# Kernel tuning notes

Hardware: AMD Instinct MI355X
Metric: run time of the kernel (lower is better)

The kernel has to match this reference:

```python
import jax, jax.numpy as jnp
import numpy as np

B, D, H, T, F = 2, 256, 8, 128, 64
C = H * F          # channels = 512
TE = 512           # time_embed_dim


def setup_inputs() -> dict:
    key = jax.random.key(0)
    ks = jax.random.split(key, 9)
    pd = jax.random.randint(ks[2], (B, T, T), 0, 2 * T - 1, dtype=jnp.int32) - (T - 1)
    s = 0.02
    return {
        "qk": jax.random.normal(ks[0], (B, D, H, T, F), jnp.float32),
        "temb": jax.random.normal(ks[1], (B, T, TE), jnp.float32),
        "pairwise_distances": pd,
        "w_dist": jax.random.normal(ks[3], (3, C), jnp.float32) * s,
        "b_dist": jax.random.normal(ks[4], (C,), jnp.float32) * s,
        "w_time": jax.random.normal(ks[5], (TE, C), jnp.float32) * s,
        "b_time": jax.random.normal(ks[6], (C,), jnp.float32) * s,
        "w_out": jax.random.normal(ks[7], (C, C), jnp.float32) * s,
        "b_out": jax.random.normal(ks[8], (C,), jnp.float32) * s,
    }


def _rpe_net(temb, pd, w_dist, b_dist, w_time, b_time, w_out, b_out):
    d = pd.astype(jnp.float32)
    # (B, T, S, 3): log(1+d+), log(1+d-), indicator(d==0)
    dist_embs = jnp.stack(
        [jnp.log1p(jnp.maximum(d, 0.0)),
         jnp.log1p(jnp.maximum(-d, 0.0)),
         (pd == 0).astype(jnp.float32)],
        axis=-1,
    )
    emb = (temb @ w_time + b_time)[:, :, None, :] + dist_embs @ w_dist + b_dist  # (B,T,S,C)
    R = jax.nn.silu(emb) @ w_out + b_out  # (B,T,S,C)
    return R.reshape(*pd.shape, H, F)     # (B,T,S,H,F)


def reference(qk, temb, pairwise_distances, w_dist, b_dist, w_time, b_time, w_out, b_out):
    R = _rpe_net(temb, pairwise_distances, w_dist, b_dist, w_time, b_time, w_out, b_out)
    # forward_qk: contract head_dim f for every (t, s) pair
    return jnp.einsum('bdhtf,btshf->bdhts', qk, R)
```

## Files before the change

kernel.cpp:

```cpp
#include <hip/hip_runtime.h>
#include <hip/hip_bf16.h>

#define B_  2
#define D_  256
#define H_  8
#define T_  128
#define S_  128
#define F_  64
#define C_  512
#define TE_ 512

typedef _Float16 f16x8 __attribute__((ext_vector_type(8)));
typedef _Float16 f16x4 __attribute__((ext_vector_type(4)));
typedef float    f32x4 __attribute__((ext_vector_type(4)));

__global__ __launch_bounds__(256) void k_time_proj(
    const float* __restrict__ temb, const float* __restrict__ w_time,
    const float* __restrict__ b_time, const float* __restrict__ b_dist,
    float* __restrict__ tp)
{
    int row0 = blockIdx.x * 2;
    int tid  = threadIdx.x;
    __shared__ float te[2][TE_];
    for (int i = tid; i < 2 * TE_; i += 256)
        te[i >> 9][i & 511] = temb[(size_t)row0 * TE_ + i];
    __syncthreads();
    for (int half = 0; half < 2; ++half) {
        int c = tid + half * 256;
        float bias = b_time[c] + b_dist[c];
        float a0 = bias, a1 = bias;
        for (int e = 0; e < TE_; ++e) {
            float w = w_time[(size_t)e * C_ + c];
            a0 += te[0][e] * w;
            a1 += te[1][e] * w;
        }
        tp[(size_t)row0 * C_ + c]       = a0;
        tp[(size_t)(row0 + 1) * C_ + c] = a1;
    }
}

__global__ __launch_bounds__(128) void k_embed_silu(
    const float* __restrict__ tp, const int* __restrict__ pd,
    const float* __restrict__ w_dist, _Float16* __restrict__ A)
{
    int row = blockIdx.x;
    int bt  = row >> 7;
    int d   = pd[row];
    float f0 = log1pf(fmaxf((float)d, 0.f));
    float f1 = log1pf(fmaxf((float)(-d), 0.f));
    float f2 = (d == 0) ? 1.f : 0.f;
    int c0 = threadIdx.x * 4;
    float4 t4 = *(const float4*)&tp[(size_t)bt * C_ + c0];
    float4 w0 = *(const float4*)&w_dist[c0];
    float4 w1 = *(const float4*)&w_dist[C_ + c0];
    float4 w2 = *(const float4*)&w_dist[2 * C_ + c0];
    float e0 = t4.x + f0 * w0.x + f1 * w1.x + f2 * w2.x;
    float e1 = t4.y + f0 * w0.y + f1 * w1.y + f2 * w2.y;
    float e2 = t4.z + f0 * w0.z + f1 * w1.z + f2 * w2.z;
    float e3 = t4.w + f0 * w0.w + f1 * w1.w + f2 * w2.w;
    f16x4 v;
    v.x = (_Float16)(e0 / (1.f + expf(-e0)));
    v.y = (_Float16)(e1 / (1.f + expf(-e1)));
    v.z = (_Float16)(e2 / (1.f + expf(-e2)));
    v.w = (_Float16)(e3 / (1.f + expf(-e3)));
    *(f16x4*)&A[(size_t)row * C_ + c0] = v;
}

__global__ __launch_bounds__(512) void k_wt(
    const float* __restrict__ w_out, _Float16* __restrict__ Wt)
{
    int n = blockIdx.x;
    int k = threadIdx.x;
    Wt[(size_t)n * C_ + k] = (_Float16)w_out[(size_t)k * C_ + n];
}

__global__ __launch_bounds__(256) void k_gemm_R(
    const _Float16* __restrict__ A, const _Float16* __restrict__ Wt,
    const float* __restrict__ b_out, _Float16* __restrict__ R)
{
    const int K = 512, N = 512;
    __shared__ _Float16 As[128][72];
    __shared__ _Float16 Bs[128][72];
    int bm = blockIdx.x, bn = blockIdx.y;
    int tid = threadIdx.x;
    int wave = tid >> 6, lane = tid & 63;
    int wm = (wave >> 1) * 64, wn = (wave & 1) * 64;
    int mrow = lane & 15, kq = (lane >> 4) * 8;
    int lrow = tid >> 3, lcol = (tid & 7) * 8;
    const size_t arow0 = (size_t)bm * 128;
    f32x4 acc[4][4] = {};
    for (int k0 = 0; k0 < K; k0 += 64) {
#pragma unroll
        for (int p = 0; p < 4; ++p) {
            int r = p * 32 + lrow;
            *(f16x8*)&As[r][lcol] = *(const f16x8*)&A[(arow0 + r) * K + k0 + lcol];
            *(f16x8*)&Bs[r][lcol] = *(const f16x8*)&Wt[(size_t)(bn * 128 + r) * K + k0 + lcol];
        }
        __syncthreads();
#pragma unroll
        for (int ks = 0; ks < 64; ks += 32) {
            f16x8 af[4], bfr[4];
#pragma unroll
            for (int i = 0; i < 4; ++i) af[i]  = *(const f16x8*)&As[wm + i * 16 + mrow][ks + kq];
#pragma unroll
            for (int j = 0; j < 4; ++j) bfr[j] = *(const f16x8*)&Bs[wn + j * 16 + mrow][ks + kq];
#pragma unroll
            for (int i = 0; i < 4; ++i)
#pragma unroll
                for (int j = 0; j < 4; ++j)
                    acc[i][j] = __builtin_amdgcn_mfma_f32_16x16x32_f16(af[i], bfr[j], acc[i][j], 0, 0, 0);
        }
        __syncthreads();
    }
    int col = lane & 15, rb = (lane >> 4) * 4;
#pragma unroll
    for (int j = 0; j < 4; ++j) {
        int n = bn * 128 + wn + j * 16 + col;
        float bo = b_out[n];
#pragma unroll
        for (int i = 0; i < 4; ++i)
#pragma unroll
            for (int r = 0; r < 4; ++r) {
                size_t m = arow0 + wm + i * 16 + rb + r;
                R[m * N + n] = (_Float16)(acc[i][j][r] + bo);
            }
    }
}

__global__ __launch_bounds__(256) void k_einsum(
    const float* __restrict__ qk, const _Float16* __restrict__ R,
    float* __restrict__ out)
{
    __shared__ _Float16 Aq[128][72];
    __shared__ _Float16 Br[128][72];
    int bht  = blockIdx.x;
    int dblk = blockIdx.y;
    int t = bht & 127;
    int h = (bht >> 7) & 7;
    int b = bht >> 10;
    int tid = threadIdx.x;
    int wave = tid >> 6, lane = tid & 63;
    int wm = (wave >> 1) * 64, wn = (wave & 1) * 64;

    const size_t qbase = (size_t)b * (D_ * H_ * T_ * F_) + (size_t)h * (T_ * F_)
                       + (size_t)t * F_ + (size_t)dblk * 128 * (H_ * T_ * F_);
    {
        int r  = tid >> 4;
        int c4 = (tid & 15) * 4;
#pragma unroll
        for (int p = 0; p < 8; ++p) {
            int row = p * 16 + r;
            float4 v = *(const float4*)&qk[qbase + (size_t)row * (H_ * T_ * F_) + c4];
            f16x4 hv;
            hv.x = (_Float16)v.x; hv.y = (_Float16)v.y;
            hv.z = (_Float16)v.z; hv.w = (_Float16)v.w;
            *(f16x4*)&Aq[row][c4] = hv;
        }
    }
    {
        const size_t rbase = ((size_t)(b * T_ + t) * S_) * C_ + h * 64;
        int r  = tid >> 3;
        int c8 = (tid & 7) * 8;
#pragma unroll
        for (int p = 0; p < 4; ++p) {
            int row = p * 32 + r;
            *(f16x8*)&Br[row][c8] = *(const f16x8*)&R[rbase + (size_t)row * C_ + c8];
        }
    }
    __syncthreads();

    int mrow = lane & 15, kq = (lane >> 4) * 8;
    f32x4 acc[4][4] = {};
#pragma unroll
    for (int ks = 0; ks < 64; ks += 32) {
        f16x8 af[4], bfr[4];
#pragma unroll
        for (int i = 0; i < 4; ++i) af[i]  = *(const f16x8*)&Aq[wm + i * 16 + mrow][ks + kq];
#pragma unroll
        for (int j = 0; j < 4; ++j) bfr[j] = *(const f16x8*)&Br[wn + j * 16 + mrow][ks + kq];
#pragma unroll
        for (int i = 0; i < 4; ++i)
#pragma unroll
            for (int j = 0; j < 4; ++j)
                acc[i][j] = __builtin_amdgcn_mfma_f32_16x16x32_f16(af[i], bfr[j], acc[i][j], 0, 0, 0);
    }

    const size_t obase = (size_t)b * (D_ * H_ * T_ * S_) + (size_t)h * (T_ * S_)
                       + (size_t)t * S_ + (size_t)dblk * 128 * (H_ * T_ * S_);
    int col = lane & 15, rb = (lane >> 4) * 4;
#pragma unroll
    for (int i = 0; i < 4; ++i)
#pragma unroll
        for (int r = 0; r < 4; ++r) {
            int dloc = wm + i * 16 + rb + r;
            size_t o = obase + (size_t)dloc * (H_ * T_ * S_);
#pragma unroll
            for (int j = 0; j < 4; ++j)
                out[o + wn + j * 16 + col] = acc[i][j][r];
        }
}

extern "C" void kernel_launch(void* const* d_in, const int* in_sizes, int n_in,
                              void* d_out, int out_size, void* d_ws, size_t ws_size,
                              hipStream_t stream) {
    (void)in_sizes; (void)n_in; (void)out_size; (void)ws_size;
    const float* qk     = (const float*)d_in[0];
    const float* temb   = (const float*)d_in[1];
    const int*   pd     = (const int*)d_in[2];
    const float* w_dist = (const float*)d_in[3];
    const float* b_dist = (const float*)d_in[4];
    const float* w_time = (const float*)d_in[5];
    const float* b_time = (const float*)d_in[6];
    const float* w_out  = (const float*)d_in[7];
    const float* b_out  = (const float*)d_in[8];
    float* out = (float*)d_out;

    char* ws = (char*)d_ws;
    float*     tp = (float*)ws;
    _Float16*  Wt = (_Float16*)(ws + 512 * 1024);
    _Float16*  A  = (_Float16*)(ws + 1024 * 1024);
    _Float16*  R  = (_Float16*)(ws + 1024 * 1024 + 33554432);

    k_time_proj<<<dim3(B_ * T_ / 2), dim3(256), 0, stream>>>(temb, w_time, b_time, b_dist, tp);
    k_wt<<<dim3(C_), dim3(C_), 0, stream>>>(w_out, Wt);
    k_embed_silu<<<dim3(B_ * T_ * S_), dim3(128), 0, stream>>>(tp, pd, w_dist, A);
    k_gemm_R<<<dim3(256, 4), dim3(256), 0, stream>>>(A, Wt, b_out, R);
    k_einsum<<<dim3(B_ * H_ * T_, 2), dim3(256), 0, stream>>>(qk, R, out);
}
```

Measured before the change: 509.0 us.

## Fuse distance embedding and SiLU into RPE GEMM, tile weight transpose, load einsum operands directly

```diff
diff --git a/kernel.cpp b/kernel.cpp
--- a/kernel.cpp
+++ b/kernel.cpp
@@ -39,62 +39,75 @@
     }
 }
 
-__global__ __launch_bounds__(128) void k_embed_silu(
+__global__ __launch_bounds__(256) void k_wt(
+    const float* __restrict__ w_out, _Float16* __restrict__ Wt)
+{
+    __shared__ float tile[64][65];
+    int bn = blockIdx.x;
+    int bk = blockIdx.y;
+    int tx = threadIdx.x & 63;
+    int ty = threadIdx.x >> 6;
+#pragma unroll
+    for (int p = 0; p < 16; ++p) {
+        int row = p * 4 + ty;
+        tile[row][tx] = w_out[(size_t)(bk * 64 + row) * C_ + bn * 64 + tx];
+    }
+    __syncthreads();
+#pragma unroll
+    for (int p = 0; p < 16; ++p) {
+        int row = p * 4 + ty;
+        Wt[(size_t)(bn * 64 + row) * C_ + bk * 64 + tx] = (_Float16)tile[tx][row];
+    }
+}
+
+__global__ __launch_bounds__(256) void k_rpe_gemm(
     const float* __restrict__ tp, const int* __restrict__ pd,
-    const float* __restrict__ w_dist, _Float16* __restrict__ A)
-{
-    int row = blockIdx.x;
-    int bt  = row >> 7;
-    int d   = pd[row];
-    float f0 = log1pf(fmaxf((float)d, 0.f));
-    float f1 = log1pf(fmaxf((float)(-d), 0.f));
-    float f2 = (d == 0) ? 1.f : 0.f;
-    int c0 = threadIdx.x * 4;
-    float4 t4 = *(const float4*)&tp[(size_t)bt * C_ + c0];
-    float4 w0 = *(const float4*)&w_dist[c0];
-    float4 w1 = *(const float4*)&w_dist[C_ + c0];
-    float4 w2 = *(const float4*)&w_dist[2 * C_ + c0];
-    float e0 = t4.x + f0 * w0.x + f1 * w1.x + f2 * w2.x;
-    float e1 = t4.y + f0 * w0.y + f1 * w1.y + f2 * w2.y;
-    float e2 = t4.z + f0 * w0.z + f1 * w1.z + f2 * w2.z;
-    float e3 = t4.w + f0 * w0.w + f1 * w1.w + f2 * w2.w;
-    f16x4 v;
-    v.x = (_Float16)(e0 / (1.f + expf(-e0)));
-    v.y = (_Float16)(e1 / (1.f + expf(-e1)));
-    v.z = (_Float16)(e2 / (1.f + expf(-e2)));
-    v.w = (_Float16)(e3 / (1.f + expf(-e3)));
-    *(f16x4*)&A[(size_t)row * C_ + c0] = v;
-}
-
-__global__ __launch_bounds__(512) void k_wt(
-    const float* __restrict__ w_out, _Float16* __restrict__ Wt)
-{
-    int n = blockIdx.x;
-    int k = threadIdx.x;
-    Wt[(size_t)n * C_ + k] = (_Float16)w_out[(size_t)k * C_ + n];
-}
-
-__global__ __launch_bounds__(256) void k_gemm_R(
-    const _Float16* __restrict__ A, const _Float16* __restrict__ Wt,
+    const float* __restrict__ w_dist, const _Float16* __restrict__ Wt,
     const float* __restrict__ b_out, _Float16* __restrict__ R)
 {
-    const int K = 512, N = 512;
     __shared__ _Float16 As[128][72];
     __shared__ _Float16 Bs[128][72];
+    __shared__ float fs[3][128];
+    __shared__ float tps[C_];
+    __shared__ float wds[3][C_];
     int bm = blockIdx.x, bn = blockIdx.y;
     int tid = threadIdx.x;
+
+    if (tid < 128) {
+        int d = pd[bm * 128 + tid];
+        fs[0][tid] = log1pf(fmaxf((float)d, 0.f));
+        fs[1][tid] = log1pf(fmaxf((float)(-d), 0.f));
+        fs[2][tid] = (d == 0) ? 1.f : 0.f;
+    }
+    for (int i = tid; i < C_; i += 256) tps[i] = tp[(size_t)bm * C_ + i];
+    for (int i = tid; i < 3 * C_; i += 256) wds[i >> 9][i & 511] = w_dist[i];
+    __syncthreads();
+
     int wave = tid >> 6, lane = tid & 63;
     int wm = (wave >> 1) * 64, wn = (wave & 1) * 64;
     int mrow = lane & 15, kq = (lane >> 4) * 8;
+    int srow  = tid >> 1;
+    int khalf = (tid & 1) * 32;
     int lrow = tid >> 3, lcol = (tid & 7) * 8;
-    const size_t arow0 = (size_t)bm * 128;
+    float f0 = fs[0][srow], f1 = fs[1][srow], f2 = fs[2][srow];
+
     f32x4 acc[4][4] = {};
-    for (int k0 = 0; k0 < K; k0 += 64) {
+    for (int k0 = 0; k0 < C_; k0 += 64) {
+        _Float16 abuf[32];
+#pragma unroll
+        for (int kk = 0; kk < 32; ++kk) {
+            int k = k0 + khalf + kk;
+            float e = tps[k] + f0 * wds[0][k] + f1 * wds[1][k] + f2 * wds[2][k];
+            e = e / (1.f + __expf(-e));
+            abuf[kk] = (_Float16)e;
+        }
+#pragma unroll
+        for (int v = 0; v < 4; ++v)
+            *(f16x8*)&As[srow][khalf + v * 8] = *(const f16x8*)&abuf[v * 8];
 #pragma unroll
         for (int p = 0; p < 4; ++p) {
             int r = p * 32 + lrow;
-            *(f16x8*)&As[r][lcol] = *(const f16x8*)&A[(arow0 + r) * K + k0 + lcol];
-            *(f16x8*)&Bs[r][lcol] = *(const f16x8*)&Wt[(size_t)(bn * 128 + r) * K + k0 + lcol];
+            *(f16x8*)&Bs[r][lcol] = *(const f16x8*)&Wt[(size_t)(bn * 128 + r) * C_ + k0 + lcol];
         }
         __syncthreads();
 #pragma unroll
@@ -113,6 +126,7 @@
         __syncthreads();
     }
     int col = lane & 15, rb = (lane >> 4) * 4;
+    const size_t arow0 = (size_t)bm * 128;
 #pragma unroll
     for (int j = 0; j < 4; ++j) {
         int n = bn * 128 + wn + j * 16 + col;
@@ -122,7 +136,7 @@
 #pragma unroll
             for (int r = 0; r < 4; ++r) {
                 size_t m = arow0 + wm + i * 16 + rb + r;
-                R[m * N + n] = (_Float16)(acc[i][j][r] + bo);
+                R[m * C_ + n] = (_Float16)(acc[i][j][r] + bo);
             }
     }
 }
@@ -131,8 +145,6 @@
     const float* __restrict__ qk, const _Float16* __restrict__ R,
     float* __restrict__ out)
 {
-    __shared__ _Float16 Aq[128][72];
-    __shared__ _Float16 Br[128][72];
     int bht  = blockIdx.x;
     int dblk = blockIdx.y;
     int t = bht & 127;
@@ -141,43 +153,32 @@
     int tid = threadIdx.x;
     int wave = tid >> 6, lane = tid & 63;
     int wm = (wave >> 1) * 64, wn = (wave & 1) * 64;
-
-    const size_t qbase = (size_t)b * (D_ * H_ * T_ * F_) + (size_t)h * (T_ * F_)
-                       + (size_t)t * F_ + (size_t)dblk * 128 * (H_ * T_ * F_);
-    {
-        int r  = tid >> 4;
-        int c4 = (tid & 15) * 4;
-#pragma unroll
-        for (int p = 0; p < 8; ++p) {
-            int row = p * 16 + r;
-            float4 v = *(const float4*)&qk[qbase + (size_t)row * (H_ * T_ * F_) + c4];
-            f16x4 hv;
-            hv.x = (_Float16)v.x; hv.y = (_Float16)v.y;
-            hv.z = (_Float16)v.z; hv.w = (_Float16)v.w;
-            *(f16x4*)&Aq[row][c4] = hv;
-        }
-    }
-    {
-        const size_t rbase = ((size_t)(b * T_ + t) * S_) * C_ + h * 64;
-        int r  = tid >> 3;
-        int c8 = (tid & 7) * 8;
-#pragma unroll
-        for (int p = 0; p < 4; ++p) {
-            int row = p * 32 + r;
-            *(f16x8*)&Br[row][c8] = *(const f16x8*)&R[rbase + (size_t)row * C_ + c8];
-        }
-    }
-    __syncthreads();
-
     int mrow = lane & 15, kq = (lane >> 4) * 8;
+
+    const size_t HTF = (size_t)H_ * T_ * F_;
+    const float* qbase = qk + (size_t)b * D_ * HTF + (size_t)h * (T_ * F_)
+                       + (size_t)t * F_ + (size_t)(dblk * 128) * HTF;
+    const _Float16* rbase = R + ((size_t)(b * T_ + t) * S_) * C_ + h * 64;
+
     f32x4 acc[4][4] = {};
 #pragma unroll
     for (int ks = 0; ks < 64; ks += 32) {
         f16x8 af[4], bfr[4];
 #pragma unroll
-        for (int i = 0; i < 4; ++i) af[i]  = *(const f16x8*)&Aq[wm + i * 16 + mrow][ks + kq];
-#pragma unroll
-        for (int j = 0; j < 4; ++j) bfr[j] = *(const f16x8*)&Br[wn + j * 16 + mrow][ks + kq];
+        for (int i = 0; i < 4; ++i) {
+            const float* p = qbase + (size_t)(wm + i * 16 + mrow) * HTF + ks + kq;
+            float4 v0 = *(const float4*)p;
+            float4 v1 = *(const float4*)(p + 4);
+            f16x8 a;
+            a[0] = (_Float16)v0.x; a[1] = (_Float16)v0.y;
+            a[2] = (_Float16)v0.z; a[3] = (_Float16)v0.w;
+            a[4] = (_Float16)v1.x; a[5] = (_Float16)v1.y;
+            a[6] = (_Float16)v1.z; a[7] = (_Float16)v1.w;
+            af[i] = a;
+        }
+#pragma unroll
+        for (int j = 0; j < 4; ++j)
+            bfr[j] = *(const f16x8*)(rbase + (size_t)(wn + j * 16 + mrow) * C_ + ks + kq);
 #pragma unroll
         for (int i = 0; i < 4; ++i)
 #pragma unroll
@@ -185,15 +186,15 @@
                 acc[i][j] = __builtin_amdgcn_mfma_f32_16x16x32_f16(af[i], bfr[j], acc[i][j], 0, 0, 0);
     }
 
-    const size_t obase = (size_t)b * (D_ * H_ * T_ * S_) + (size_t)h * (T_ * S_)
-                       + (size_t)t * S_ + (size_t)dblk * 128 * (H_ * T_ * S_);
+    const size_t obase = (size_t)b * ((size_t)D_ * H_ * T_ * S_) + (size_t)h * (T_ * S_)
+                       + (size_t)t * S_ + (size_t)(dblk * 128) * ((size_t)H_ * T_ * S_);
     int col = lane & 15, rb = (lane >> 4) * 4;
 #pragma unroll
     for (int i = 0; i < 4; ++i)
 #pragma unroll
         for (int r = 0; r < 4; ++r) {
             int dloc = wm + i * 16 + rb + r;
-            size_t o = obase + (size_t)dloc * (H_ * T_ * S_);
+            size_t o = obase + (size_t)dloc * ((size_t)H_ * T_ * S_);
 #pragma unroll
             for (int j = 0; j < 4; ++j)
                 out[o + wn + j * 16 + col] = acc[i][j][r];
@@ -218,12 +219,10 @@
     char* ws = (char*)d_ws;
     float*     tp = (float*)ws;
     _Float16*  Wt = (_Float16*)(ws + 512 * 1024);
-    _Float16*  A  = (_Float16*)(ws + 1024 * 1024);
-    _Float16*  R  = (_Float16*)(ws + 1024 * 1024 + 33554432);
+    _Float16*  R  = (_Float16*)(ws + 1024 * 1024);
 
     k_time_proj<<<dim3(B_ * T_ / 2), dim3(256), 0, stream>>>(temb, w_time, b_time, b_dist, tp);
-    k_wt<<<dim3(C_), dim3(C_), 0, stream>>>(w_out, Wt);
-    k_embed_silu<<<dim3(B_ * T_ * S_), dim3(128), 0, stream>>>(tp, pd, w_dist, A);
-    k_gemm_R<<<dim3(256, 4), dim3(256), 0, stream>>>(A, Wt, b_out, R);
+    k_wt<<<dim3(8, 8), dim3(256), 0, stream>>>(w_out, Wt);
+    k_rpe_gemm<<<dim3(256, 4), dim3(256), 0, stream>>>(tp, pd, w_dist, Wt, b_out, R);
     k_einsum<<<dim3(B_ * H_ * T_, 2), dim3(256), 0, stream>>>(qk, R, out);
 }
```

Result: slower. 541.8 us (+6.4%).
